# Performance work log

Measured on AMD Instinct MI355X. Metric: run time of the kernel, lower is better.

## Reference

```python
import jax, jax.numpy as jnp
import numpy as np

N_NODES = 100000
N_FEAT = 512
N_CLASS = 40
N_EDGES = 3200000


def setup_inputs() -> dict:
    key = jax.random.key(0)
    k1, k2, k3 = jax.random.split(key, 3)
    x = jax.random.normal(k1, (N_NODES, N_FEAT), dtype=jnp.float32)
    edge_index = jax.random.randint(k2, (2, N_EDGES), 0, N_NODES, dtype=jnp.int64)
    # GCNConv linear weight (glorot) and bias (zeros in PyG default)
    limit = float(np.sqrt(6.0 / (N_FEAT + N_CLASS)))
    W = jax.random.uniform(k3, (N_FEAT, N_CLASS), dtype=jnp.float32,
                           minval=-limit, maxval=limit)
    b = jnp.zeros((N_CLASS,), dtype=jnp.float32)
    return {"x": x, "edge_index": edge_index, "W": W, "b": b}


def reference(x, edge_index, W, b):
    N = x.shape[0]
    # Linear transform first (PyG GCNConv does lin() before propagate)
    h = x @ W  # [N, nclass]
    # Add self-loops
    loops = jnp.arange(N, dtype=edge_index.dtype)
    src = jnp.concatenate([edge_index[0], loops])
    dst = jnp.concatenate([edge_index[1], loops])
    # Symmetric normalization: deg computed on destination nodes (incl. self-loops)
    ones = jnp.ones_like(dst, dtype=h.dtype)
    deg = jax.ops.segment_sum(ones, dst, num_segments=N)  # [N]
    dinv = jnp.where(deg > 0, jax.lax.rsqrt(deg), 0.0)
    norm = dinv[src] * dinv[dst]  # [E+N]
    # Gather messages, scale, scatter-add to destinations
    msgs = h[src] * norm[:, None]  # [E+N, nclass]
    out = jax.ops.segment_sum(msgs, dst, num_segments=N) + b  # [N, nclass]
    return jax.nn.log_softmax(out, axis=1)
```

## Files before the change

### kernel.cpp

```cpp
#include <hip/hip_runtime.h>

#define WS_CNT      0u
#define WS_ROWSTART 400128u
#define WS_CURSOR   800256u
#define WS_DINV     1200384u
#define WS_BSUM     1600512u
#define WS_BOFF     1602560u
#define WS_FLAG     1604608u
#define WS_G        1604864u
#define WS_CSR      (WS_G + 16000000u)

static __global__ void k_detect(const int* __restrict__ ei, int* __restrict__ flag) {
    if (blockIdx.x == 0 && threadIdx.x == 0) {
        int allz = 1;
        for (int t = 1; t < 256; t += 2) {
            if (ei[t] != 0) { allz = 0; break; }
        }
        *flag = allz;
    }
}

static __global__ void k_deg(const int* __restrict__ ei, int E,
                             const int* __restrict__ flag, int* __restrict__ cnt) {
    const int is64 = *flag;
    int e = blockIdx.x * blockDim.x + threadIdx.x;
    const int stride = gridDim.x * blockDim.x;
    if (is64) {
        for (; e < E; e += stride) atomicAdd(&cnt[ei[2 * (E + e)]], 1);
    } else {
        for (; e < E; e += stride) atomicAdd(&cnt[ei[E + e]], 1);
    }
}

static __global__ void k_scanA(const int* __restrict__ cnt, int n, int* __restrict__ bsum) {
    __shared__ int lds[256];
    const int i = blockIdx.x * 256 + threadIdx.x;
    lds[threadIdx.x] = (i < n) ? cnt[i] : 0;
    __syncthreads();
    for (int s = 128; s > 0; s >>= 1) {
        if ((int)threadIdx.x < s) lds[threadIdx.x] += lds[threadIdx.x + s];
        __syncthreads();
    }
    if (threadIdx.x == 0) bsum[blockIdx.x] = lds[0];
}

static __global__ void k_scanB(const int* __restrict__ bsum, int nb, int* __restrict__ boff) {
    __shared__ int lds[512];
    const int t = threadIdx.x;
    const int v = (t < nb) ? bsum[t] : 0;
    lds[t] = v;
    __syncthreads();
    for (int s = 1; s < 512; s <<= 1) {
        int add = (t >= s) ? lds[t - s] : 0;
        __syncthreads();
        lds[t] += add;
        __syncthreads();
    }
    if (t < nb) boff[t] = lds[t] - v;
}

static __global__ void k_scanC(const int* __restrict__ cnt, int n, const int* __restrict__ boff,
                               int* __restrict__ rowstart, int* __restrict__ cursor) {
    __shared__ int lds[256];
    const int t = threadIdx.x;
    const int i = blockIdx.x * 256 + t;
    const int v = (i < n) ? cnt[i] : 0;
    lds[t] = v;
    __syncthreads();
    for (int s = 1; s < 256; s <<= 1) {
        int add = (t >= s) ? lds[t - s] : 0;
        __syncthreads();
        lds[t] += add;
        __syncthreads();
    }
    if (i < n) {
        const int ex = boff[blockIdx.x] + lds[t] - v;
        rowstart[i] = ex;
        cursor[i]   = ex;
    }
}

static __global__ void k_dinv(const int* __restrict__ cnt, int n, float* __restrict__ dinv) {
    const int i = blockIdx.x * blockDim.x + threadIdx.x;
    if (i < n) dinv[i] = rsqrtf((float)(cnt[i] + 1));
}

static __global__ void k_fill(const int* __restrict__ ei, int E,
                              const int* __restrict__ flag,
                              int* __restrict__ cursor, int* __restrict__ csr) {
    const int is64 = *flag;
    int e = blockIdx.x * blockDim.x + threadIdx.x;
    const int stride = gridDim.x * blockDim.x;
    if (is64) {
        for (; e < E; e += stride) {
            const int s = ei[2 * e];
            const int d = ei[2 * (E + e)];
            const int pos = atomicAdd(&cursor[d], 1);
            csr[pos] = s;
        }
    } else {
        for (; e < E; e += stride) {
            const int s = ei[e];
            const int d = ei[E + e];
            const int pos = atomicAdd(&cursor[d], 1);
            csr[pos] = s;
        }
    }
}

static __global__ __launch_bounds__(256) void k_h(const float* __restrict__ x,
                                                  const float* __restrict__ W,
                                                  const float* __restrict__ dinv,
                                                  float* __restrict__ g, int n) {
    const int row = blockIdx.x * 256 + threadIdx.x;
    if (row >= n) return;
    float acc[40];
#pragma unroll
    for (int c = 0; c < 40; ++c) acc[c] = 0.f;
    const float* xr = x + (size_t)row * 512;
    for (int k = 0; k < 512; k += 4) {
        const float4 xv = *reinterpret_cast<const float4*>(xr + k);
        const float xs[4] = {xv.x, xv.y, xv.z, xv.w};
#pragma unroll
        for (int j = 0; j < 4; ++j) {
            const float* wr = W + (size_t)(k + j) * 40;
#pragma unroll
            for (int c = 0; c < 40; ++c) acc[c] = fmaf(xs[j], wr[c], acc[c]);
        }
    }
    const float dv = dinv[row];
    float* gr = g + (size_t)row * 40;
#pragma unroll
    for (int c = 0; c < 40; c += 4) {
        float4 o;
        o.x = acc[c + 0] * dv;
        o.y = acc[c + 1] * dv;
        o.z = acc[c + 2] * dv;
        o.w = acc[c + 3] * dv;
        *reinterpret_cast<float4*>(gr + c) = o;
    }
}

static __global__ __launch_bounds__(256) void k_gather(const float* __restrict__ g,
                                                       const int* __restrict__ csr,
                                                       const int* __restrict__ rowstart,
                                                       const int* __restrict__ cnt,
                                                       const float* __restrict__ dinv,
                                                       const float* __restrict__ b,
                                                       float* __restrict__ out, int n) {
    const int t = threadIdx.x;
    if (t >= 240) return;
    const int local = t / 40;
    const int c = t - local * 40;
    const int i = blockIdx.x * 6 + local;
    if (i >= n) return;

    float acc = g[(size_t)i * 40 + c];
    const int s0 = rowstart[i];
    const int e1 = s0 + cnt[i];
    int p = s0;
    for (; p + 4 <= e1; p += 4) {
        const int sa = csr[p + 0];
        const int sb = csr[p + 1];
        const int sc = csr[p + 2];
        const int sd = csr[p + 3];
        float va = g[(size_t)sa * 40 + c];
        float vb = g[(size_t)sb * 40 + c];
        float vc = g[(size_t)sc * 40 + c];
        float vd = g[(size_t)sd * 40 + c];
        acc += va; acc += vb; acc += vc; acc += vd;
    }
    for (; p < e1; ++p) acc += g[(size_t)csr[p] * 40 + c];

    out[(size_t)i * 40 + c] = acc * dinv[i] + b[c];
}

static __global__ void k_lsm(float* __restrict__ out, int n) {
    const int i = blockIdx.x * blockDim.x + threadIdx.x;
    if (i >= n) return;
    float* r = out + (size_t)i * 40;
    float v[40];
#pragma unroll
    for (int c = 0; c < 40; c += 4) {
        const float4 t4 = *reinterpret_cast<const float4*>(r + c);
        v[c] = t4.x; v[c + 1] = t4.y; v[c + 2] = t4.z; v[c + 3] = t4.w;
    }
    float m = v[0];
#pragma unroll
    for (int c = 1; c < 40; ++c) m = fmaxf(m, v[c]);
    float s = 0.f;
#pragma unroll
    for (int c = 0; c < 40; ++c) s += __expf(v[c] - m);
    const float l = m + __logf(s);
#pragma unroll
    for (int c = 0; c < 40; c += 4) {
        float4 o;
        o.x = v[c + 0] - l;
        o.y = v[c + 1] - l;
        o.z = v[c + 2] - l;
        o.w = v[c + 3] - l;
        *reinterpret_cast<float4*>(r + c) = o;
    }
}

extern "C" void kernel_launch(void* const* d_in, const int* in_sizes, int n_in,
                              void* d_out, int out_size, void* d_ws, size_t ws_size,
                              hipStream_t stream) {
    const float* x  = (const float*)d_in[0];
    const int*   ei = (const int*)d_in[1];
    const float* W  = (const float*)d_in[2];
    const float* b  = (const float*)d_in[3];
    float* out = (float*)d_out;

    const int N = in_sizes[0] / 512;
    const int E = in_sizes[1] / 2;

    char* ws = (char*)d_ws;
    int*   cnt      = (int*)(ws + WS_CNT);
    int*   rowstart = (int*)(ws + WS_ROWSTART);
    int*   cursor   = (int*)(ws + WS_CURSOR);
    float* dinv     = (float*)(ws + WS_DINV);
    int*   bsum     = (int*)(ws + WS_BSUM);
    int*   boff     = (int*)(ws + WS_BOFF);
    int*   flag     = (int*)(ws + WS_FLAG);
    float* g        = (float*)(ws + WS_G);
    int*   csr      = (int*)(ws + WS_CSR);

    const int NB = (N + 255) / 256;

    hipMemsetAsync(cnt, 0, (size_t)N * sizeof(int), stream);
    k_detect<<<1, 64, 0, stream>>>(ei, flag);
    k_deg<<<2048, 256, 0, stream>>>(ei, E, flag, cnt);
    k_scanA<<<NB, 256, 0, stream>>>(cnt, N, bsum);
    k_scanB<<<1, 512, 0, stream>>>(bsum, NB, boff);
    k_scanC<<<NB, 256, 0, stream>>>(cnt, N, boff, rowstart, cursor);
    k_dinv<<<NB, 256, 0, stream>>>(cnt, N, dinv);
    k_fill<<<2048, 256, 0, stream>>>(ei, E, flag, cursor, csr);
    k_h<<<NB, 256, 0, stream>>>(x, W, dinv, g, N);
    k_gather<<<(N + 5) / 6, 256, 0, stream>>>(g, csr, rowstart, cnt, dinv, b, out, N);
    k_lsm<<<NB, 256, 0, stream>>>(out, N);
}
```

Before: 625.4 us.

## Replace per-node CSR build with coarse 256-node bucket sort and LDS accumulation

Replaces the exact per-destination CSR construction (global atomics on 100K counters, three-pass scan, global cursor atomics) with a two-pass bucket sort into 391 buckets of 256 destination nodes. Each entry packs the source and the local destination into one word. Degrees are computed per bucket in LDS, and the gather kernel accumulates messages with LDS float atomics per bucket, with log-softmax fused into its epilogue. This cuts global atomic contention and kernel count. The cost is LDS atomic traffic and only 391 large gather blocks, which may underuse the GPU. The 17-bit source packing assumes N below 131072.

```diff
diff --git a/kernel.cpp b/kernel.cpp
--- a/kernel.cpp
+++ b/kernel.cpp
@@ -1,14 +1,15 @@
 #include <hip/hip_runtime.h>
 
-#define WS_CNT      0u
-#define WS_ROWSTART 400128u
-#define WS_CURSOR   800256u
-#define WS_DINV     1200384u
-#define WS_BSUM     1600512u
-#define WS_BOFF     1602560u
-#define WS_FLAG     1604608u
-#define WS_G        1604864u
-#define WS_CSR      (WS_G + 16000000u)
+#define NBUK   391
+#define CHUNK  3072
+
+#define WS_FLAG   0u
+#define WS_GCNT   1024u
+#define WS_GSTART 4096u
+#define WS_GCUR   8192u
+#define WS_DINV   16384u
+#define WS_G      425984u
+#define WS_BUCK   16425984u
 
 static __global__ void k_detect(const int* __restrict__ ei, int* __restrict__ flag) {
     if (blockIdx.x == 0 && threadIdx.x == 0) {
@@ -20,92 +21,127 @@
     }
 }
 
-static __global__ void k_deg(const int* __restrict__ ei, int E,
-                             const int* __restrict__ flag, int* __restrict__ cnt) {
+static __global__ __launch_bounds__(512) void k_bcount(const int* __restrict__ ei, int E,
+                                                       const int* __restrict__ flag,
+                                                       int* __restrict__ gcnt) {
+    __shared__ int h[NBUK];
+    const int t = threadIdx.x;
+    for (int b = t; b < NBUK; b += 512) h[b] = 0;
+    __syncthreads();
     const int is64 = *flag;
-    int e = blockIdx.x * blockDim.x + threadIdx.x;
-    const int stride = gridDim.x * blockDim.x;
+    const int i0 = blockIdx.x * CHUNK;
+    const int i1 = min(E, i0 + CHUNK);
     if (is64) {
-        for (; e < E; e += stride) atomicAdd(&cnt[ei[2 * (E + e)]], 1);
+        for (int e = i0 + t; e < i1; e += 512) atomicAdd(&h[ei[2 * (E + e)] >> 8], 1);
     } else {
-        for (; e < E; e += stride) atomicAdd(&cnt[ei[E + e]], 1);
-    }
-}
-
-static __global__ void k_scanA(const int* __restrict__ cnt, int n, int* __restrict__ bsum) {
-    __shared__ int lds[256];
-    const int i = blockIdx.x * 256 + threadIdx.x;
-    lds[threadIdx.x] = (i < n) ? cnt[i] : 0;
-    __syncthreads();
-    for (int s = 128; s > 0; s >>= 1) {
-        if ((int)threadIdx.x < s) lds[threadIdx.x] += lds[threadIdx.x + s];
-        __syncthreads();
-    }
-    if (threadIdx.x == 0) bsum[blockIdx.x] = lds[0];
-}
-
-static __global__ void k_scanB(const int* __restrict__ bsum, int nb, int* __restrict__ boff) {
+        for (int e = i0 + t; e < i1; e += 512) atomicAdd(&h[ei[E + e] >> 8], 1);
+    }
+    __syncthreads();
+    for (int b = t; b < NBUK; b += 512)
+        if (h[b]) atomicAdd(&gcnt[b], h[b]);
+}
+
+static __global__ void k_bscan(const int* __restrict__ gcnt, int* __restrict__ gstart,
+                               int* __restrict__ gcur) {
     __shared__ int lds[512];
     const int t = threadIdx.x;
-    const int v = (t < nb) ? bsum[t] : 0;
+    const int v = (t < NBUK) ? gcnt[t] : 0;
     lds[t] = v;
     __syncthreads();
     for (int s = 1; s < 512; s <<= 1) {
-        int add = (t >= s) ? lds[t - s] : 0;
-        __syncthreads();
-        lds[t] += add;
-        __syncthreads();
-    }
-    if (t < nb) boff[t] = lds[t] - v;
-}
-
-static __global__ void k_scanC(const int* __restrict__ cnt, int n, const int* __restrict__ boff,
-                               int* __restrict__ rowstart, int* __restrict__ cursor) {
-    __shared__ int lds[256];
+        const int a = (t >= s) ? lds[t - s] : 0;
+        __syncthreads();
+        lds[t] += a;
+        __syncthreads();
+    }
+    if (t < NBUK) { gstart[t] = lds[t] - v; gcur[t] = lds[t] - v; }
+}
+
+static __global__ __launch_bounds__(512) void k_scatter(const int* __restrict__ ei, int E,
+                                                        const int* __restrict__ flag,
+                                                        int* __restrict__ gcur,
+                                                        unsigned* __restrict__ buck) {
+    __shared__ int hist[NBUK];
+    __shared__ int lofs[NBUK];
+    __shared__ int base[NBUK];
+    __shared__ int cur[NBUK];
+    __shared__ int sc[512];
+    __shared__ unsigned stag[CHUNK];
+    __shared__ unsigned short bkt[CHUNK];
+
     const int t = threadIdx.x;
-    const int i = blockIdx.x * 256 + t;
-    const int v = (i < n) ? cnt[i] : 0;
-    lds[t] = v;
-    __syncthreads();
-    for (int s = 1; s < 256; s <<= 1) {
-        int add = (t >= s) ? lds[t - s] : 0;
-        __syncthreads();
-        lds[t] += add;
-        __syncthreads();
-    }
-    if (i < n) {
-        const int ex = boff[blockIdx.x] + lds[t] - v;
-        rowstart[i] = ex;
-        cursor[i]   = ex;
-    }
-}
-
-static __global__ void k_dinv(const int* __restrict__ cnt, int n, float* __restrict__ dinv) {
-    const int i = blockIdx.x * blockDim.x + threadIdx.x;
-    if (i < n) dinv[i] = rsqrtf((float)(cnt[i] + 1));
-}
-
-static __global__ void k_fill(const int* __restrict__ ei, int E,
-                              const int* __restrict__ flag,
-                              int* __restrict__ cursor, int* __restrict__ csr) {
     const int is64 = *flag;
-    int e = blockIdx.x * blockDim.x + threadIdx.x;
-    const int stride = gridDim.x * blockDim.x;
+    const int i0 = blockIdx.x * CHUNK;
+    const int i1 = min(E, i0 + CHUNK);
+    const int nloc = i1 - i0;
+
+    for (int b = t; b < NBUK; b += 512) hist[b] = 0;
+    __syncthreads();
+
     if (is64) {
-        for (; e < E; e += stride) {
+        for (int e = i0 + t; e < i1; e += 512) atomicAdd(&hist[ei[2 * (E + e)] >> 8], 1);
+    } else {
+        for (int e = i0 + t; e < i1; e += 512) atomicAdd(&hist[ei[E + e] >> 8], 1);
+    }
+    __syncthreads();
+
+    sc[t] = (t < NBUK) ? hist[t] : 0;
+    __syncthreads();
+    for (int s = 1; s < 512; s <<= 1) {
+        const int a = (t >= s) ? sc[t - s] : 0;
+        __syncthreads();
+        sc[t] += a;
+        __syncthreads();
+    }
+    if (t < NBUK) {
+        lofs[t] = sc[t] - hist[t];
+        base[t] = hist[t] ? atomicAdd(&gcur[t], hist[t]) : 0;
+        cur[t]  = 0;
+    }
+    __syncthreads();
+
+    if (is64) {
+        for (int e = i0 + t; e < i1; e += 512) {
             const int s = ei[2 * e];
             const int d = ei[2 * (E + e)];
-            const int pos = atomicAdd(&cursor[d], 1);
-            csr[pos] = s;
+            const int b = d >> 8;
+            const int l = atomicAdd(&cur[b], 1);
+            const int p = lofs[b] + l;
+            stag[p] = (unsigned)s | ((unsigned)(d & 255) << 17);
+            bkt[p]  = (unsigned short)b;
         }
     } else {
-        for (; e < E; e += stride) {
+        for (int e = i0 + t; e < i1; e += 512) {
             const int s = ei[e];
             const int d = ei[E + e];
-            const int pos = atomicAdd(&cursor[d], 1);
-            csr[pos] = s;
-        }
-    }
+            const int b = d >> 8;
+            const int l = atomicAdd(&cur[b], 1);
+            const int p = lofs[b] + l;
+            stag[p] = (unsigned)s | ((unsigned)(d & 255) << 17);
+            bkt[p]  = (unsigned short)b;
+        }
+    }
+    __syncthreads();
+
+    for (int j = t; j < nloc; j += 512) {
+        const int b = bkt[j];
+        buck[(size_t)base[b] + (j - lofs[b])] = stag[j];
+    }
+}
+
+static __global__ __launch_bounds__(256) void k_bdeg(const unsigned* __restrict__ buck,
+                                                     const int* __restrict__ gstart,
+                                                     const int* __restrict__ gcnt,
+                                                     float* __restrict__ dinv, int N) {
+    __shared__ int h[256];
+    const int b = blockIdx.x, t = threadIdx.x;
+    h[t] = 0;
+    __syncthreads();
+    const int s0 = gstart[b], n = gcnt[b];
+    for (int j = t; j < n; j += 256) atomicAdd(&h[buck[s0 + j] >> 17], 1);
+    __syncthreads();
+    const int node = b * 256 + t;
+    if (node < N) dinv[node] = rsqrtf((float)(h[t] + 1));
 }
 
 static __global__ __launch_bounds__(256) void k_h(const float* __restrict__ x,
@@ -141,65 +177,65 @@
     }
 }
 
-static __global__ __launch_bounds__(256) void k_gather(const float* __restrict__ g,
-                                                       const int* __restrict__ csr,
-                                                       const int* __restrict__ rowstart,
-                                                       const int* __restrict__ cnt,
+static __global__ __launch_bounds__(512) void k_gather(const float* __restrict__ g,
+                                                       const unsigned* __restrict__ buck,
+                                                       const int* __restrict__ gstart,
+                                                       const int* __restrict__ gcnt,
                                                        const float* __restrict__ dinv,
-                                                       const float* __restrict__ b,
-                                                       float* __restrict__ out, int n) {
-    const int t = threadIdx.x;
-    if (t >= 240) return;
-    const int local = t / 40;
-    const int c = t - local * 40;
-    const int i = blockIdx.x * 6 + local;
-    if (i >= n) return;
-
-    float acc = g[(size_t)i * 40 + c];
-    const int s0 = rowstart[i];
-    const int e1 = s0 + cnt[i];
-    int p = s0;
-    for (; p + 4 <= e1; p += 4) {
-        const int sa = csr[p + 0];
-        const int sb = csr[p + 1];
-        const int sc = csr[p + 2];
-        const int sd = csr[p + 3];
-        float va = g[(size_t)sa * 40 + c];
-        float vb = g[(size_t)sb * 40 + c];
-        float vc = g[(size_t)sc * 40 + c];
-        float vd = g[(size_t)sd * 40 + c];
-        acc += va; acc += vb; acc += vc; acc += vd;
-    }
-    for (; p < e1; ++p) acc += g[(size_t)csr[p] * 40 + c];
-
-    out[(size_t)i * 40 + c] = acc * dinv[i] + b[c];
-}
-
-static __global__ void k_lsm(float* __restrict__ out, int n) {
-    const int i = blockIdx.x * blockDim.x + threadIdx.x;
-    if (i >= n) return;
-    float* r = out + (size_t)i * 40;
-    float v[40];
-#pragma unroll
-    for (int c = 0; c < 40; c += 4) {
-        const float4 t4 = *reinterpret_cast<const float4*>(r + c);
-        v[c] = t4.x; v[c + 1] = t4.y; v[c + 2] = t4.z; v[c + 3] = t4.w;
-    }
-    float m = v[0];
-#pragma unroll
-    for (int c = 1; c < 40; ++c) m = fmaxf(m, v[c]);
-    float s = 0.f;
-#pragma unroll
-    for (int c = 0; c < 40; ++c) s += __expf(v[c] - m);
-    const float l = m + __logf(s);
-#pragma unroll
-    for (int c = 0; c < 40; c += 4) {
-        float4 o;
-        o.x = v[c + 0] - l;
-        o.y = v[c + 1] - l;
-        o.z = v[c + 2] - l;
-        o.w = v[c + 3] - l;
-        *reinterpret_cast<float4*>(r + c) = o;
+                                                       const float* __restrict__ bias,
+                                                       float* __restrict__ out, int N) {
+    __shared__ float acc[256][41];
+    const int b = blockIdx.x, t = threadIdx.x;
+    const int nbase = b * 256;
+    const int nloc = min(256, N - nbase);
+
+    for (int idx = t; idx < nloc * 40; idx += 512) {
+        const int r = idx / 40, c = idx - r * 40;
+        acc[r][c] = g[(size_t)(nbase + r) * 40 + c];
+    }
+    __syncthreads();
+
+    const int s0 = gstart[b], n = gcnt[b];
+    for (int j = t; j < n; j += 512) {
+        const unsigned pay = buck[s0 + j];
+        const int src = (int)(pay & 0x1FFFFu);
+        const int dl  = (int)(pay >> 17);
+        const float* gr = g + (size_t)src * 40;
+#pragma unroll
+        for (int c = 0; c < 40; c += 4) {
+            const float4 v = *reinterpret_cast<const float4*>(gr + c);
+            atomicAdd(&acc[dl][c + 0], v.x);
+            atomicAdd(&acc[dl][c + 1], v.y);
+            atomicAdd(&acc[dl][c + 2], v.z);
+            atomicAdd(&acc[dl][c + 3], v.w);
+        }
+    }
+    __syncthreads();
+
+    if (t < nloc) {
+        const int node = nbase + t;
+        const float dv = dinv[node];
+        float v[40];
+        float m = -1e30f;
+#pragma unroll
+        for (int c = 0; c < 40; ++c) {
+            v[c] = acc[t][c] * dv + bias[c];
+            m = fmaxf(m, v[c]);
+        }
+        float s = 0.f;
+#pragma unroll
+        for (int c = 0; c < 40; ++c) s += __expf(v[c] - m);
+        const float l = m + __logf(s);
+        float* r = out + (size_t)node * 40;
+#pragma unroll
+        for (int c = 0; c < 40; c += 4) {
+            float4 o;
+            o.x = v[c + 0] - l;
+            o.y = v[c + 1] - l;
+            o.z = v[c + 2] - l;
+            o.w = v[c + 3] - l;
+            *reinterpret_cast<float4*>(r + c) = o;
+        }
     }
 }
 
@@ -216,27 +252,23 @@
     const int E = in_sizes[1] / 2;
 
     char* ws = (char*)d_ws;
-    int*   cnt      = (int*)(ws + WS_CNT);
-    int*   rowstart = (int*)(ws + WS_ROWSTART);
-    int*   cursor   = (int*)(ws + WS_CURSOR);
-    float* dinv     = (float*)(ws + WS_DINV);
-    int*   bsum     = (int*)(ws + WS_BSUM);
-    int*   boff     = (int*)(ws + WS_BOFF);
-    int*   flag     = (int*)(ws + WS_FLAG);
-    float* g        = (float*)(ws + WS_G);
-    int*   csr      = (int*)(ws + WS_CSR);
-
-    const int NB = (N + 255) / 256;
-
-    hipMemsetAsync(cnt, 0, (size_t)N * sizeof(int), stream);
+    int*      flag   = (int*)(ws + WS_FLAG);
+    int*      gcnt   = (int*)(ws + WS_GCNT);
+    int*      gstart = (int*)(ws + WS_GSTART);
+    int*      gcur   = (int*)(ws + WS_GCUR);
+    float*    dinv   = (float*)(ws + WS_DINV);
+    float*    g      = (float*)(ws + WS_G);
+    unsigned* buck   = (unsigned*)(ws + WS_BUCK);
+
+    const int NB   = (N + 255) / 256;
+    const int NEB  = (E + CHUNK - 1) / CHUNK;
+
+    hipMemsetAsync(gcnt, 0, NBUK * sizeof(int), stream);
     k_detect<<<1, 64, 0, stream>>>(ei, flag);
-    k_deg<<<2048, 256, 0, stream>>>(ei, E, flag, cnt);
-    k_scanA<<<NB, 256, 0, stream>>>(cnt, N, bsum);
-    k_scanB<<<1, 512, 0, stream>>>(bsum, NB, boff);
-    k_scanC<<<NB, 256, 0, stream>>>(cnt, N, boff, rowstart, cursor);
-    k_dinv<<<NB, 256, 0, stream>>>(cnt, N, dinv);
-    k_fill<<<2048, 256, 0, stream>>>(ei, E, flag, cursor, csr);
+    k_bcount<<<NEB, 512, 0, stream>>>(ei, E, flag, gcnt);
+    k_bscan<<<1, 512, 0, stream>>>(gcnt, gstart, gcur);
+    k_scatter<<<NEB, 512, 0, stream>>>(ei, E, flag, gcur, buck);
+    k_bdeg<<<NBUK, 256, 0, stream>>>(buck, gstart, gcnt, dinv, N);
     k_h<<<NB, 256, 0, stream>>>(x, W, dinv, g, N);
-    k_gather<<<(N + 5) / 6, 256, 0, stream>>>(g, csr, rowstart, cnt, dinv, b, out, N);
-    k_lsm<<<NB, 256, 0, stream>>>(out, N);
-}
+    k_gather<<<NBUK, 512, 0, stream>>>(g, buck, gstart, gcnt, dinv, b, out, N);
+}
```

New measurement: 1.066 ms. 1.71x slower.
